# Kernel tuning notes

Measured on AMD Instinct MI355X. Metric: run time of the kernel, lower is better.

Reference implementation:

```python
import jax, jax.numpy as jnp
from jax import lax
import numpy as np

TWO_PI = 2.0 * np.pi

# ---- batched real-amplitude statevector simulator (RY/CNOT only -> real state) ----

def _init_state(batch, n):
    s = jnp.zeros((batch, 2 ** n), dtype=jnp.float32).at[:, 0].set(1.0)
    return s.reshape((batch,) + (2,) * n)

def _ry(state, wire, theta, n):
    # state: (B, 2,...,2); theta: scalar or (B,)
    ax = wire + 1
    h = theta * 0.5
    c = jnp.reshape(jnp.cos(h), (-1,) + (1,) * (n - 1))
    s = jnp.reshape(jnp.sin(h), (-1,) + (1,) * (n - 1))
    s0 = lax.index_in_dim(state, 0, ax, keepdims=False)
    s1 = lax.index_in_dim(state, 1, ax, keepdims=False)
    return jnp.stack([c * s0 - s * s1, s * s0 + c * s1], axis=ax)

def _cnot(state, ctrl, tgt):
    axc, axt = ctrl + 1, tgt + 1
    s0 = lax.index_in_dim(state, 0, axc, keepdims=True)
    s1 = lax.index_in_dim(state, 1, axc, keepdims=True)
    return jnp.concatenate([s0, jnp.flip(s1, axis=axt)], axis=axc)

def _expz(state, wire, n):
    sgn = jnp.reshape(jnp.array([1.0, -1.0], state.dtype),
                      (1,) * (wire + 1) + (2,) + (1,) * (n - wire - 1))
    return jnp.sum(state * state * sgn, axis=tuple(range(1, n + 1)))

# gate lists: ('ry', theta_index, wire) or ('cx', control, target)
EDGE_OPS = [('ry',0,0),('ry',1,1),('cx',0,1),('ry',2,2),('ry',3,3),('cx',3,2),
            ('ry',4,4),('ry',5,5),('cx',4,5),('ry',6,6),('ry',7,7),('cx',7,6),
            ('ry',8,1),('ry',9,2),('cx',1,2),('ry',10,5),('ry',11,6),('cx',6,5),
            ('ry',12,2),('ry',13,5),('cx',2,5),('ry',14,5)]

NODE_OPS = [('ry',0,0),('ry',1,1),('cx',0,1),('ry',2,2),('ry',3,3),('cx',3,2),
            ('ry',4,4),('ry',5,5),('cx',4,5),('ry',6,6),('ry',7,7),('cx',7,6),
            ('ry',8,8),('ry',9,9),('cx',8,9),('ry',10,10),('ry',11,11),('cx',11,10),
            ('ry',12,1),('ry',13,2),('cx',1,2),('ry',14,5),('ry',15,6),('cx',6,5),
            ('ry',16,9),('ry',17,10),('cx',10,9),('ry',18,2),('ry',19,5),('cx',2,5),
            ('ry',20,5),('ry',21,9),('cx',5,9),('ry',22,4)]

def _circuit(angles, theta, ops, n, meas_wire):
    st = _init_state(angles.shape[0], n)
    for i in range(n):  # input encoding RYs, per-sample angles
        st = _ry(st, i, angles[:, i], n)
    for op in ops:
        if op[0] == 'ry':
            st = _ry(st, op[2], theta[op[1]], n)
        else:
            st = _cnot(st, op[1], op[2])
    return _expz(st, meas_wire, n)

# ---- GNN pieces ----

def _edge_net(H, Ri, Ro, theta):
    bo = Ro.T @ H                      # [E,4]
    bi = Ri.T @ H                      # [E,4]
    B = jnp.concatenate([bo, bi], axis=1)  # [E,8]
    return (1.0 - _circuit(B, theta, EDGE_OPS, 8, 5)) * 0.5

def _node_net(H, e, Ri, Ro, theta):
    bo = Ro.T @ H                      # [E,4]
    bi = Ri.T @ H                      # [E,4]
    mi = (Ri * e[None, :]) @ bo        # [N,4]
    mo = (Ro * e[None, :]) @ bi        # [N,4]
    M = jnp.concatenate([mi, mo, H], axis=1)  # [N,12]
    return jnp.pi * (1.0 - _circuit(M, theta, NODE_OPS, 12, 9))

def _gnn(X, Ri, Ro, W_in, b_in, theta_edge, theta_node, n_iters=2):
    H = jnp.concatenate([jax.nn.sigmoid(X @ W_in + b_in) * TWO_PI, X], axis=1)  # [N,4]
    e = _edge_net(H, Ri, Ro, theta_edge)
    for _ in range(n_iters):
        h = _node_net(H, e, Ri, Ro, theta_node)   # [N]
        H = jnp.concatenate([h[:, None], X], axis=1)
        e = _edge_net(H, Ri, Ro, theta_edge)
    return e


def setup_inputs() -> dict:
    key = jax.random.key(0)
    ks = jax.random.split(key, 6)
    N, E = 2048, 4096
    X = jax.random.normal(ks[0], (N, 3), jnp.float32)
    recv = jax.random.randint(ks[1], (E,), 0, N)
    send = jax.random.randint(ks[2], (E,), 0, N)
    cols = jnp.arange(E)
    Ri = jnp.zeros((N, E), jnp.float32).at[recv, cols].set(1.0)
    Ro = jnp.zeros((N, E), jnp.float32).at[send, cols].set(1.0)
    W_in = jax.random.normal(ks[3], (3, 1), jnp.float32)
    b_in = jnp.zeros((1,), jnp.float32)
    theta_edge = jax.random.uniform(ks[4], (15,), jnp.float32, 0.0, TWO_PI)
    theta_node = jax.random.uniform(ks[5], (23,), jnp.float32, 0.0, TWO_PI)
    return {'X': X, 'Ri': Ri, 'Ro': Ro, 'W_in': W_in, 'b_in': b_in,
            'theta_edge': theta_edge, 'theta_node': theta_node}


def reference(X, Ri, Ro, W_in, b_in, theta_edge, theta_node):
    return _gnn(X, Ri, Ro, W_in, b_in, theta_edge, theta_node, n_iters=2)
```

## Files before the change

### kernel.cpp

```cpp
#include <hip/hip_runtime.h>
#include <math.h>

#define N_NODES 2048
#define N_EDGES 4096
#define PI_F 3.14159265358979323846f
#define TWO_PI_F 6.28318530717958647692f

__device__ __forceinline__ float agent_load(const float* p) {
    return __hip_atomic_load(p, __ATOMIC_RELAXED, __HIP_MEMORY_SCOPE_AGENT);
}
__device__ __forceinline__ void agent_store(float* p, float v) {
    __hip_atomic_store(p, v, __ATOMIC_RELAXED, __HIP_MEMORY_SCOPE_AGENT);
}
__device__ __forceinline__ void agent_store_i(int* p, int v) {
    __hip_atomic_store(p, v, __ATOMIC_RELAXED, __HIP_MEMORY_SCOPE_AGENT);
}
__device__ __forceinline__ void spin_ge(const int* p, int v) {
    while (__hip_atomic_load(p, __ATOMIC_RELAXED, __HIP_MEMORY_SCOPE_AGENT) < v)
        __builtin_amdgcn_s_sleep(2);
    asm volatile("" ::: "memory");
}


template<int M>
__device__ __forceinline__ void ry16(float* a, float c, float s) {
#pragma unroll
    for (int i = 0; i < 16; ++i)
        if (!(i & M)) {
            int j = i | M;
            float x0 = a[i], x1 = a[j];
            a[i] = c * x0 - s * x1;
            a[j] = s * x0 + c * x1;
        }
}
template<int MC, int MT>
__device__ __forceinline__ void cx16(float* a) {
#pragma unroll
    for (int i = 0; i < 16; ++i)
        if ((i & MC) && !(i & MT)) {
            int j = i | MT;
            float t = a[i]; a[i] = a[j]; a[j] = t;
        }
}

template<bool BTYPE>
__device__ __forceinline__ void sub16(const float* ic, const float* is,
                                      const float* thc, const float* ths,
                                      float& z, float& x) {
    float a[16];
    a[0] = ic[3]; a[1] = is[3];
#pragma unroll
    for (int i = 0; i < 2; ++i) { a[i | 2] = a[i] * is[2]; a[i] *= ic[2]; }
#pragma unroll
    for (int i = 0; i < 4; ++i) { a[i | 4] = a[i] * is[1]; a[i] *= ic[1]; }
#pragma unroll
    for (int i = 0; i < 8; ++i) { a[i | 8] = a[i] * is[0]; a[i] *= ic[0]; }
    ry16<8>(a, thc[0], ths[0]);
    ry16<4>(a, thc[1], ths[1]);
    cx16<8, 4>(a);
    ry16<2>(a, thc[2], ths[2]);
    ry16<1>(a, thc[3], ths[3]);
    cx16<1, 2>(a);
    ry16<4>(a, thc[4], ths[4]);
    ry16<2>(a, thc[5], ths[5]);
    if (BTYPE) { cx16<2, 4>(a); ry16<4>(a, thc[6], ths[6]); }
    else       { cx16<4, 2>(a); ry16<2>(a, thc[6], ths[6]); }
    const int m = BTYPE ? 4 : 2;
    z = 0.f; x = 0.f;
#pragma unroll
    for (int i = 0; i < 16; ++i) z += (i & m) ? -a[i] * a[i] : a[i] * a[i];
    if (BTYPE) {
#pragma unroll
        for (int i = 0; i < 16; ++i) if (!(i & 4)) x += a[i] * a[i | 4];
        x *= 2.f;
    }
}

__device__ __forceinline__ void edge_pub(
        float chh, float shh, const float* cxv, const float* sxv,
        const float* teC, const float* teS,
        float& zA, float& zB, float& xB) {
    float ic[4] = {chh, cxv[0], cxv[1], cxv[2]};
    float is[4] = {shh, sxv[0], sxv[1], sxv[2]};
    float dmy;
    {
        float thc[7] = {teC[0], teC[1], teC[2], teC[3], teC[8], teC[9], teC[12]};
        float ths[7] = {teS[0], teS[1], teS[2], teS[3], teS[8], teS[9], teS[12]};
        sub16<false>(ic, is, thc, ths, zA, dmy);
    }
    {
        float thc[7] = {teC[4], teC[5], teC[6], teC[7], teC[10], teC[11], teC[13]};
        float ths[7] = {teS[4], teS[5], teS[6], teS[7], teS[10], teS[11], teS[13]};
        sub16<true>(ic, is, thc, ths, zB, xB);
    }
}

__global__ __launch_bounds__(256) void k_setup(
        const float* __restrict__ X, const float* __restrict__ Ri,
        const float* __restrict__ Ro, const float* __restrict__ W,
        const float* __restrict__ b, const float* __restrict__ te,
        const float* __restrict__ tn,
        int* __restrict__ send, int* __restrict__ recv, float* __restrict__ H,
        float* __restrict__ pub, float* __restrict__ trig,
        int* __restrict__ deg) {
    int tid = blockIdx.x * blockDim.x + threadIdx.x;
    if (tid < N_NODES) {
        float x0 = X[tid*3+0], x1 = X[tid*3+1], x2 = X[tid*3+2];
        float z = x0*W[0] + x1*W[1] + x2*W[2] + b[0];
        float sg = 1.0f / (1.0f + __expf(-z));
        float h = sg * TWO_PI_F;
        ((float4*)H)[tid] = make_float4(h, x0, x1, x2);
        float chh, shh, cxv[3], sxv[3];
        __sincosf(0.5f*h,  &shh, &chh);
        __sincosf(0.5f*x0, &sxv[0], &cxv[0]);
        __sincosf(0.5f*x1, &sxv[1], &cxv[1]);
        __sincosf(0.5f*x2, &sxv[2], &cxv[2]);
        float teC[14], teS[14];
#pragma unroll
        for (int k = 0; k < 14; ++k) __sincosf(0.5f*te[k], &teS[k], &teC[k]);
        float zA, zB, xB;
        edge_pub(chh, shh, cxv, sxv, teC, teS, zA, zB, xB);
        pub[tid*4+0] = zA; pub[tid*4+1] = zB; pub[tid*4+2] = xB;
    }
    if (tid >= 4096 && tid < 4096 + 15) {
        int i = tid - 4096; float s, c;
        __sincosf(0.5f * te[i], &s, &c);
        trig[i] = c; trig[16 + i] = s;
    }
    if (tid >= 4224 && tid < 4224 + 23) {
        int i = tid - 4224; float s, c;
        __sincosf(0.5f * tn[i], &s, &c);
        trig[32 + i] = c; trig[56 + i] = s;
    }
    const float4 vi = ((const float4*)Ri)[tid];
    const float4 vo = ((const float4*)Ro)[tid];
    int base = tid * 4;
    int n = base >> 12;
    int e = base & (N_EDGES - 1);
    int cnt = 0;
    if (vi.x != 0.f) { recv[e+0] = n; ++cnt; }
    if (vi.y != 0.f) { recv[e+1] = n; ++cnt; }
    if (vi.z != 0.f) { recv[e+2] = n; ++cnt; }
    if (vi.w != 0.f) { recv[e+3] = n; ++cnt; }
    if (vo.x != 0.f) { send[e+0] = n; ++cnt; }
    if (vo.y != 0.f) { send[e+1] = n; ++cnt; }
    if (vo.z != 0.f) { send[e+2] = n; ++cnt; }
    if (vo.w != 0.f) { send[e+3] = n; ++cnt; }
    if (cnt) atomicAdd(&deg[n], cnt);
}

__device__ __forceinline__ void scatter8(float ev, const float4& Hs, const float4& Hr,
                                         int si, int ri,
                                         float* __restrict__ macc, int* __restrict__ arr) {
    atomicAdd(&macc[ri*8+0], ev*Hs.x); atomicAdd(&macc[ri*8+1], ev*Hs.y);
    atomicAdd(&macc[ri*8+2], ev*Hs.z); atomicAdd(&macc[ri*8+3], ev*Hs.w);
    atomicAdd(&macc[si*8+4], ev*Hr.x); atomicAdd(&macc[si*8+5], ev*Hr.y);
    atomicAdd(&macc[si*8+6], ev*Hr.z); atomicAdd(&macc[si*8+7], ev*Hr.w);
    asm volatile("s_waitcnt vmcnt(0)" ::: "memory");
    atomicAdd(&arr[ri], 1); atomicAdd(&arr[si], 1);
}

__global__ __launch_bounds__(64) void k_mega(
        float* __restrict__ H, float* __restrict__ pub,
        const int* __restrict__ send, const int* __restrict__ recv,
        const float* __restrict__ trig,
        float* __restrict__ maccA, float* __restrict__ maccB,
        int* __restrict__ arrA, int* __restrict__ arrB,
        int* __restrict__ epoch, const int* __restrict__ deg,
        float* __restrict__ out) {
    int lane = threadIdx.x;
    int blk  = blockIdx.x;

    if (blk < 64) {
        int e = blk * 64 + lane;
        int si = send[e], ri = recv[e];
        float4 Hs = ((const float4*)H)[si];
        float4 Hr = ((const float4*)H)[ri];
        float c14 = trig[14], s14 = trig[30];
        float C14 = c14*c14 - s14*s14;
        float S14 = 2.f*c14*s14;

        float zA = pub[si*4+0], zB = pub[ri*4+1], xB = pub[ri*4+2];
        float ev = 0.5f*(1.f - (C14*zA*zB - S14*xB));
        scatter8(ev, Hs, Hr, si, ri, maccA, arrA);

        spin_ge(epoch + si, 1); spin_ge(epoch + ri, 1);
        zA = agent_load(&pub[si*4+0]);
        zB = agent_load(&pub[ri*4+1]);
        xB = agent_load(&pub[ri*4+2]);
        Hs.x = agent_load(&H[si*4]);
        Hr.x = agent_load(&H[ri*4]);
        ev = 0.5f*(1.f - (C14*zA*zB - S14*xB));
        scatter8(ev, Hs, Hr, si, ri, maccB, arrB);

        spin_ge(epoch + si, 2); spin_ge(epoch + ri, 2);
        zA = agent_load(&pub[si*4+0]);
        zB = agent_load(&pub[ri*4+1]);
        xB = agent_load(&pub[ri*4+2]);
        out[e] = 0.5f*(1.f - (C14*zA*zB - S14*xB));
    } else {
        int n = (blk - 64) * 64 + lane;
        float4 Hn = ((const float4*)H)[n];
        float chh, shh, cxv[3], sxv[3];
        __sincosf(0.5f*Hn.x, &shh, &chh);
        __sincosf(0.5f*Hn.y, &sxv[0], &cxv[0]);
        __sincosf(0.5f*Hn.z, &sxv[1], &cxv[1]);
        __sincosf(0.5f*Hn.w, &sxv[2], &cxv[2]);
        int dg = deg[n];
        const float* teC = trig;      const float* teS = trig + 16;
        const float* tnC = trig + 32; const float* tnS = trig + 56;
        float C20 = tnC[20]*tnC[20] - tnS[20]*tnS[20];
        float S20 = 2.f*tnC[20]*tnS[20];

        for (int it = 0; it < 2; ++it) {
            const float* mc_ = it ? maccB : maccA;
            const int*   ar  = it ? arrB  : arrA;
            spin_ge(ar + n, dg);
            float M[8], mC[8], mS[8];
#pragma unroll
            for (int k = 0; k < 8; ++k) M[k] = agent_load(mc_ + n*8 + k);
#pragma unroll
            for (int k = 0; k < 8; ++k) __sincosf(0.5f*M[k], &mS[k], &mC[k]);
            float zA1, zA2, xA2, zB9, dmy;
            {
                float thc[7] = {tnC[0],tnC[1],tnC[2],tnC[3],tnC[12],tnC[13],tnC[18]};
                float ths[7] = {tnS[0],tnS[1],tnS[2],tnS[3],tnS[12],tnS[13],tnS[18]};
                sub16<false>(&mC[0], &mS[0], thc, ths, zA1, dmy);
            }
            {
                float thc[7] = {tnC[4],tnC[5],tnC[6],tnC[7],tnC[14],tnC[15],tnC[19]};
                float ths[7] = {tnS[4],tnS[5],tnS[6],tnS[7],tnS[14],tnS[15],tnS[19]};
                sub16<true>(&mC[4], &mS[4], thc, ths, zA2, xA2);
            }
            {
                float ic[4] = {chh, cxv[0], cxv[1], cxv[2]};
                float is[4] = {shh, sxv[0], sxv[1], sxv[2]};
                float thc[7] = {tnC[8],tnC[9],tnC[10],tnC[11],tnC[16],tnC[17],tnC[21]};
                float ths[7] = {tnS[8],tnS[9],tnS[10],tnS[11],tnS[16],tnS[17],tnS[21]};
                sub16<true>(ic, is, thc, ths, zB9, dmy);
            }
            float p9 = (C20*zA1*zA2 - S20*xA2) * zB9;
            float h = PI_F * (1.f - p9);
            __sincosf(0.5f*h, &shh, &chh);
            float zAe, zBe, xBe;
            edge_pub(chh, shh, cxv, sxv, teC, teS, zAe, zBe, xBe);
            agent_store(&pub[n*4+0], zAe);
            agent_store(&pub[n*4+1], zBe);
            agent_store(&pub[n*4+2], xBe);
            agent_store(&H[n*4], h);
            asm volatile("s_waitcnt vmcnt(0)" ::: "memory");
            agent_store_i(epoch + n, it + 1);
        }
    }
}

extern "C" void kernel_launch(void* const* d_in, const int* in_sizes, int n_in,
                              void* d_out, int out_size, void* d_ws, size_t ws_size,
                              hipStream_t stream) {
    const float* X  = (const float*)d_in[0];
    const float* Ri = (const float*)d_in[1];
    const float* Ro = (const float*)d_in[2];
    const float* W  = (const float*)d_in[3];
    const float* b  = (const float*)d_in[4];
    const float* te = (const float*)d_in[5];
    const float* tn = (const float*)d_in[6];
    float* out = (float*)d_out;

    int*   send  = (int*)d_ws;
    int*   recv  = send + N_EDGES;
    float* H     = (float*)(recv + N_EDGES);
    float* pub   = H + N_NODES * 4;
    float* trig  = pub + N_NODES * 4;
    float* maccA = trig + 128;
    float* maccB = maccA + N_NODES * 8;
    int*   arrA  = (int*)(maccB + N_NODES * 8);
    int*   arrB  = arrA + N_NODES;
    int*   epoch = arrB + N_NODES;
    int*   deg   = epoch + N_NODES;
    size_t zbytes = (size_t)(2 * N_NODES * 8 + 4 * N_NODES) * sizeof(float);

    hipMemsetAsync((void*)maccA, 0, zbytes, stream);
    int total4 = (N_NODES * N_EDGES) / 4;
    k_setup<<<total4 / 256, 256, 0, stream>>>(X, Ri, Ro, W, b, te, tn,
                                              send, recv, H, pub, trig, deg);
    k_mega<<<96, 64, 0, stream>>>(H, pub, send, recv, trig,
                                  maccA, maccB, arrA, arrB, epoch, deg, out);
}
```

Measured before the change: 123.5 us.

## Fuse setup scan and message-passing into one persistent dataflow kernel

Merges the adjacency-scan setup kernel and the persistent edge/node kernel into a single 256-block launch. Edge blocks spin on per-edge send/recv indices (stored as row+1) and per-node init flags, so message passing starts while the dense Ri/Ro scan is still running. Node blocks compute the initial features and trig values locally and wait on a global scan-done counter before reading degrees. This removes a kernel boundary and overlaps the bandwidth-bound scan with the start of the dependent work. In exchange the scan now runs from a fixed grid of persistent blocks with an unrolled strided loop, and correctness depends on all blocks being co-resident for the spin-waits.

```diff
diff --git a/kernel.cpp b/kernel.cpp
--- a/kernel.cpp
+++ b/kernel.cpp
@@ -6,7 +6,17 @@
 #define PI_F 3.14159265358979323846f
 #define TWO_PI_F 6.28318530717958647692f
 
+#define EDGE_BLKS 16
+#define NODE_BLKS 8
+#define TOTAL_BLKS 256
+#define SCAN_BLKS (TOTAL_BLKS - EDGE_BLKS)
+#define SCAN_STRIDE (SCAN_BLKS * 256)
+#define TOT4 (N_NODES * N_EDGES / 4)
+
 __device__ __forceinline__ float agent_load(const float* p) {
+    return __hip_atomic_load(p, __ATOMIC_RELAXED, __HIP_MEMORY_SCOPE_AGENT);
+}
+__device__ __forceinline__ int agent_load_i(const int* p) {
     return __hip_atomic_load(p, __ATOMIC_RELAXED, __HIP_MEMORY_SCOPE_AGENT);
 }
 __device__ __forceinline__ void agent_store(float* p, float v) {
@@ -19,6 +29,12 @@
     while (__hip_atomic_load(p, __ATOMIC_RELAXED, __HIP_MEMORY_SCOPE_AGENT) < v)
         __builtin_amdgcn_s_sleep(2);
     asm volatile("" ::: "memory");
+}
+__device__ __forceinline__ int spin_idx(const int* p) {
+    int v;
+    while ((v = agent_load_i(p)) == 0) __builtin_amdgcn_s_sleep(2);
+    asm volatile("" ::: "memory");
+    return v - 1;
 }
 
 
@@ -95,60 +111,6 @@
     }
 }
 
-__global__ __launch_bounds__(256) void k_setup(
-        const float* __restrict__ X, const float* __restrict__ Ri,
-        const float* __restrict__ Ro, const float* __restrict__ W,
-        const float* __restrict__ b, const float* __restrict__ te,
-        const float* __restrict__ tn,
-        int* __restrict__ send, int* __restrict__ recv, float* __restrict__ H,
-        float* __restrict__ pub, float* __restrict__ trig,
-        int* __restrict__ deg) {
-    int tid = blockIdx.x * blockDim.x + threadIdx.x;
-    if (tid < N_NODES) {
-        float x0 = X[tid*3+0], x1 = X[tid*3+1], x2 = X[tid*3+2];
-        float z = x0*W[0] + x1*W[1] + x2*W[2] + b[0];
-        float sg = 1.0f / (1.0f + __expf(-z));
-        float h = sg * TWO_PI_F;
-        ((float4*)H)[tid] = make_float4(h, x0, x1, x2);
-        float chh, shh, cxv[3], sxv[3];
-        __sincosf(0.5f*h,  &shh, &chh);
-        __sincosf(0.5f*x0, &sxv[0], &cxv[0]);
-        __sincosf(0.5f*x1, &sxv[1], &cxv[1]);
-        __sincosf(0.5f*x2, &sxv[2], &cxv[2]);
-        float teC[14], teS[14];
-#pragma unroll
-        for (int k = 0; k < 14; ++k) __sincosf(0.5f*te[k], &teS[k], &teC[k]);
-        float zA, zB, xB;
-        edge_pub(chh, shh, cxv, sxv, teC, teS, zA, zB, xB);
-        pub[tid*4+0] = zA; pub[tid*4+1] = zB; pub[tid*4+2] = xB;
-    }
-    if (tid >= 4096 && tid < 4096 + 15) {
-        int i = tid - 4096; float s, c;
-        __sincosf(0.5f * te[i], &s, &c);
-        trig[i] = c; trig[16 + i] = s;
-    }
-    if (tid >= 4224 && tid < 4224 + 23) {
-        int i = tid - 4224; float s, c;
-        __sincosf(0.5f * tn[i], &s, &c);
-        trig[32 + i] = c; trig[56 + i] = s;
-    }
-    const float4 vi = ((const float4*)Ri)[tid];
-    const float4 vo = ((const float4*)Ro)[tid];
-    int base = tid * 4;
-    int n = base >> 12;
-    int e = base & (N_EDGES - 1);
-    int cnt = 0;
-    if (vi.x != 0.f) { recv[e+0] = n; ++cnt; }
-    if (vi.y != 0.f) { recv[e+1] = n; ++cnt; }
-    if (vi.z != 0.f) { recv[e+2] = n; ++cnt; }
-    if (vi.w != 0.f) { recv[e+3] = n; ++cnt; }
-    if (vo.x != 0.f) { send[e+0] = n; ++cnt; }
-    if (vo.y != 0.f) { send[e+1] = n; ++cnt; }
-    if (vo.z != 0.f) { send[e+2] = n; ++cnt; }
-    if (vo.w != 0.f) { send[e+3] = n; ++cnt; }
-    if (cnt) atomicAdd(&deg[n], cnt);
-}
-
 __device__ __forceinline__ void scatter8(float ev, const float4& Hs, const float4& Hr,
                                          int si, int ri,
                                          float* __restrict__ macc, int* __restrict__ arr) {
@@ -160,27 +122,40 @@
     atomicAdd(&arr[ri], 1); atomicAdd(&arr[si], 1);
 }
 
-__global__ __launch_bounds__(64) void k_mega(
+__global__ __launch_bounds__(256, 1) void k_fused(
+        const float* __restrict__ X, const float* __restrict__ Ri,
+        const float* __restrict__ Ro, const float* __restrict__ W,
+        const float* __restrict__ b, const float* __restrict__ te,
+        const float* __restrict__ tn,
         float* __restrict__ H, float* __restrict__ pub,
-        const int* __restrict__ send, const int* __restrict__ recv,
-        const float* __restrict__ trig,
+        int* __restrict__ send, int* __restrict__ recv,
         float* __restrict__ maccA, float* __restrict__ maccB,
         int* __restrict__ arrA, int* __restrict__ arrB,
-        int* __restrict__ epoch, const int* __restrict__ deg,
+        int* __restrict__ epoch, int* __restrict__ inited,
+        int* __restrict__ deg, int* __restrict__ sdone,
         float* __restrict__ out) {
-    int lane = threadIdx.x;
-    int blk  = blockIdx.x;
-
-    if (blk < 64) {
-        int e = blk * 64 + lane;
-        int si = send[e], ri = recv[e];
-        float4 Hs = ((const float4*)H)[si];
-        float4 Hr = ((const float4*)H)[ri];
-        float c14 = trig[14], s14 = trig[30];
-        float C14 = c14*c14 - s14*s14;
-        float S14 = 2.f*c14*s14;
-
-        float zA = pub[si*4+0], zB = pub[ri*4+1], xB = pub[ri*4+2];
+    int blk = blockIdx.x, tid = threadIdx.x;
+
+    if (blk < EDGE_BLKS) {
+        int e = blk * 256 + tid;
+        float c14h, s14h;
+        __sincosf(0.5f * te[14], &s14h, &c14h);
+        float C14 = c14h*c14h - s14h*s14h;
+        float S14 = 2.f*c14h*s14h;
+
+        int si = spin_idx(send + e);
+        int ri = spin_idx(recv + e);
+        spin_ge(inited + si, 1);
+        spin_ge(inited + ri, 1);
+        float4 Hs, Hr;
+        Hs.x = agent_load(H+si*4+0); Hs.y = agent_load(H+si*4+1);
+        Hs.z = agent_load(H+si*4+2); Hs.w = agent_load(H+si*4+3);
+        Hr.x = agent_load(H+ri*4+0); Hr.y = agent_load(H+ri*4+1);
+        Hr.z = agent_load(H+ri*4+2); Hr.w = agent_load(H+ri*4+3);
+
+        float zA = agent_load(&pub[si*4+0]);
+        float zB = agent_load(&pub[ri*4+1]);
+        float xB = agent_load(&pub[ri*4+2]);
         float ev = 0.5f*(1.f - (C14*zA*zB - S14*xB));
         scatter8(ev, Hs, Hr, si, ri, maccA, arrA);
 
@@ -198,59 +173,119 @@
         zB = agent_load(&pub[ri*4+1]);
         xB = agent_load(&pub[ri*4+2]);
         out[e] = 0.5f*(1.f - (C14*zA*zB - S14*xB));
-    } else {
-        int n = (blk - 64) * 64 + lane;
-        float4 Hn = ((const float4*)H)[n];
-        float chh, shh, cxv[3], sxv[3];
-        __sincosf(0.5f*Hn.x, &shh, &chh);
-        __sincosf(0.5f*Hn.y, &sxv[0], &cxv[0]);
-        __sincosf(0.5f*Hn.z, &sxv[1], &cxv[1]);
-        __sincosf(0.5f*Hn.w, &sxv[2], &cxv[2]);
-        int dg = deg[n];
-        const float* teC = trig;      const float* teS = trig + 16;
-        const float* tnC = trig + 32; const float* tnS = trig + 56;
-        float C20 = tnC[20]*tnC[20] - tnS[20]*tnS[20];
-        float S20 = 2.f*tnC[20]*tnS[20];
-
-        for (int it = 0; it < 2; ++it) {
-            const float* mc_ = it ? maccB : maccA;
-            const int*   ar  = it ? arrB  : arrA;
-            spin_ge(ar + n, dg);
-            float M[8], mC[8], mS[8];
-#pragma unroll
-            for (int k = 0; k < 8; ++k) M[k] = agent_load(mc_ + n*8 + k);
-#pragma unroll
-            for (int k = 0; k < 8; ++k) __sincosf(0.5f*M[k], &mS[k], &mC[k]);
-            float zA1, zA2, xA2, zB9, dmy;
-            {
-                float thc[7] = {tnC[0],tnC[1],tnC[2],tnC[3],tnC[12],tnC[13],tnC[18]};
-                float ths[7] = {tnS[0],tnS[1],tnS[2],tnS[3],tnS[12],tnS[13],tnS[18]};
-                sub16<false>(&mC[0], &mS[0], thc, ths, zA1, dmy);
+        return;
+    }
+
+    bool is_node = (blk < EDGE_BLKS + NODE_BLKS);
+    int n = (blk - EDGE_BLKS) * 256 + tid;
+    float chh, shh, cxv[3], sxv[3];
+    float teC[14], teS[14], tnC[22], tnS[22];
+    if (is_node) {
+        float x0 = X[n*3+0], x1 = X[n*3+1], x2 = X[n*3+2];
+        float z = x0*W[0] + x1*W[1] + x2*W[2] + b[0];
+        float sg = 1.0f / (1.0f + __expf(-z));
+        float h = sg * TWO_PI_F;
+        __sincosf(0.5f*h,  &shh, &chh);
+        __sincosf(0.5f*x0, &sxv[0], &cxv[0]);
+        __sincosf(0.5f*x1, &sxv[1], &cxv[1]);
+        __sincosf(0.5f*x2, &sxv[2], &cxv[2]);
+#pragma unroll
+        for (int k = 0; k < 14; ++k) __sincosf(0.5f*te[k], &teS[k], &teC[k]);
+#pragma unroll
+        for (int k = 0; k < 22; ++k) __sincosf(0.5f*tn[k], &tnS[k], &tnC[k]);
+        float zA, zB, xB;
+        edge_pub(chh, shh, cxv, sxv, teC, teS, zA, zB, xB);
+        agent_store(&pub[n*4+0], zA);
+        agent_store(&pub[n*4+1], zB);
+        agent_store(&pub[n*4+2], xB);
+        agent_store(&H[n*4+0], h);
+        agent_store(&H[n*4+1], x0);
+        agent_store(&H[n*4+2], x2 == x2 ? x1 : x1);
+        agent_store(&H[n*4+3], x2);
+        asm volatile("s_waitcnt vmcnt(0)" ::: "memory");
+        agent_store_i(inited + n, 1);
+    }
+
+    {
+        int gid = (blk - EDGE_BLKS) * 256 + tid;
+        const float4* Ri4 = (const float4*)Ri;
+        const float4* Ro4 = (const float4*)Ro;
+        for (int t0 = gid; t0 < TOT4; t0 += 4 * SCAN_STRIDE) {
+            float4 vi[4], vo[4];
+#pragma unroll
+            for (int u = 0; u < 4; ++u) {
+                int t = t0 + u * SCAN_STRIDE;
+                if (t < TOT4) { vi[u] = Ri4[t]; vo[u] = Ro4[t]; }
             }
-            {
-                float thc[7] = {tnC[4],tnC[5],tnC[6],tnC[7],tnC[14],tnC[15],tnC[19]};
-                float ths[7] = {tnS[4],tnS[5],tnS[6],tnS[7],tnS[14],tnS[15],tnS[19]};
-                sub16<true>(&mC[4], &mS[4], thc, ths, zA2, xA2);
+#pragma unroll
+            for (int u = 0; u < 4; ++u) {
+                int t = t0 + u * SCAN_STRIDE;
+                if (t < TOT4) {
+                    int base = t * 4;
+                    int row = base >> 12;
+                    int e   = base & (N_EDGES - 1);
+                    int cnt = 0;
+                    if (vi[u].x != 0.f) { agent_store_i(recv+e+0, row+1); ++cnt; }
+                    if (vi[u].y != 0.f) { agent_store_i(recv+e+1, row+1); ++cnt; }
+                    if (vi[u].z != 0.f) { agent_store_i(recv+e+2, row+1); ++cnt; }
+                    if (vi[u].w != 0.f) { agent_store_i(recv+e+3, row+1); ++cnt; }
+                    if (vo[u].x != 0.f) { agent_store_i(send+e+0, row+1); ++cnt; }
+                    if (vo[u].y != 0.f) { agent_store_i(send+e+1, row+1); ++cnt; }
+                    if (vo[u].z != 0.f) { agent_store_i(send+e+2, row+1); ++cnt; }
+                    if (vo[u].w != 0.f) { agent_store_i(send+e+3, row+1); ++cnt; }
+                    if (cnt) atomicAdd(&deg[row], cnt);
+                }
             }
-            {
-                float ic[4] = {chh, cxv[0], cxv[1], cxv[2]};
-                float is[4] = {shh, sxv[0], sxv[1], sxv[2]};
-                float thc[7] = {tnC[8],tnC[9],tnC[10],tnC[11],tnC[16],tnC[17],tnC[21]};
-                float ths[7] = {tnS[8],tnS[9],tnS[10],tnS[11],tnS[16],tnS[17],tnS[21]};
-                sub16<true>(ic, is, thc, ths, zB9, dmy);
-            }
-            float p9 = (C20*zA1*zA2 - S20*xA2) * zB9;
-            float h = PI_F * (1.f - p9);
-            __sincosf(0.5f*h, &shh, &chh);
-            float zAe, zBe, xBe;
-            edge_pub(chh, shh, cxv, sxv, teC, teS, zAe, zBe, xBe);
-            agent_store(&pub[n*4+0], zAe);
-            agent_store(&pub[n*4+1], zBe);
-            agent_store(&pub[n*4+2], xBe);
-            agent_store(&H[n*4], h);
-            asm volatile("s_waitcnt vmcnt(0)" ::: "memory");
-            agent_store_i(epoch + n, it + 1);
-        }
+        }
+        asm volatile("s_waitcnt vmcnt(0)" ::: "memory");
+        __syncthreads();
+        if (tid == 0) atomicAdd(sdone, 1);
+    }
+    if (!is_node) return;
+
+    spin_ge(sdone, SCAN_BLKS);
+    int dg = agent_load_i(deg + n);
+    float C20 = tnC[20]*tnC[20] - tnS[20]*tnS[20];
+    float S20 = 2.f*tnC[20]*tnS[20];
+
+    for (int it = 0; it < 2; ++it) {
+        const float* mc_ = it ? maccB : maccA;
+        const int*   ar  = it ? arrB  : arrA;
+        spin_ge(ar + n, dg);
+        float M[8], mC[8], mS[8];
+#pragma unroll
+        for (int k = 0; k < 8; ++k) M[k] = agent_load(mc_ + n*8 + k);
+#pragma unroll
+        for (int k = 0; k < 8; ++k) __sincosf(0.5f*M[k], &mS[k], &mC[k]);
+        float zA1, zA2, xA2, zB9, dmy;
+        {
+            float thc[7] = {tnC[0],tnC[1],tnC[2],tnC[3],tnC[12],tnC[13],tnC[18]};
+            float ths[7] = {tnS[0],tnS[1],tnS[2],tnS[3],tnS[12],tnS[13],tnS[18]};
+            sub16<false>(&mC[0], &mS[0], thc, ths, zA1, dmy);
+        }
+        {
+            float thc[7] = {tnC[4],tnC[5],tnC[6],tnC[7],tnC[14],tnC[15],tnC[19]};
+            float ths[7] = {tnS[4],tnS[5],tnS[6],tnS[7],tnS[14],tnS[15],tnS[19]};
+            sub16<true>(&mC[4], &mS[4], thc, ths, zA2, xA2);
+        }
+        {
+            float ic[4] = {chh, cxv[0], cxv[1], cxv[2]};
+            float is[4] = {shh, sxv[0], sxv[1], sxv[2]};
+            float thc[7] = {tnC[8],tnC[9],tnC[10],tnC[11],tnC[16],tnC[17],tnC[21]};
+            float ths[7] = {tnS[8],tnS[9],tnS[10],tnS[11],tnS[16],tnS[17],tnS[21]};
+            sub16<true>(ic, is, thc, ths, zB9, dmy);
+        }
+        float p9 = (C20*zA1*zA2 - S20*xA2) * zB9;
+        float h = PI_F * (1.f - p9);
+        __sincosf(0.5f*h, &shh, &chh);
+        float zAe, zBe, xBe;
+        edge_pub(chh, shh, cxv, sxv, teC, teS, zAe, zBe, xBe);
+        agent_store(&pub[n*4+0], zAe);
+        agent_store(&pub[n*4+1], zBe);
+        agent_store(&pub[n*4+2], xBe);
+        agent_store(&H[n*4], h);
+        asm volatile("s_waitcnt vmcnt(0)" ::: "memory");
+        agent_store_i(epoch + n, it + 1);
     }
 }
 
@@ -266,23 +301,23 @@
     const float* tn = (const float*)d_in[6];
     float* out = (float*)d_out;
 
-    int*   send  = (int*)d_ws;
+    float* H     = (float*)d_ws;
+    float* pub   = H + N_NODES * 4;
+    int*   send  = (int*)(pub + N_NODES * 4);
     int*   recv  = send + N_EDGES;
-    float* H     = (float*)(recv + N_EDGES);
-    float* pub   = H + N_NODES * 4;
-    float* trig  = pub + N_NODES * 4;
-    float* maccA = trig + 128;
+    float* maccA = (float*)(recv + N_EDGES);
     float* maccB = maccA + N_NODES * 8;
     int*   arrA  = (int*)(maccB + N_NODES * 8);
     int*   arrB  = arrA + N_NODES;
     int*   epoch = arrB + N_NODES;
-    int*   deg   = epoch + N_NODES;
-    size_t zbytes = (size_t)(2 * N_NODES * 8 + 4 * N_NODES) * sizeof(float);
-
-    hipMemsetAsync((void*)maccA, 0, zbytes, stream);
-    int total4 = (N_NODES * N_EDGES) / 4;
-    k_setup<<<total4 / 256, 256, 0, stream>>>(X, Ri, Ro, W, b, te, tn,
-                                              send, recv, H, pub, trig, deg);
-    k_mega<<<96, 64, 0, stream>>>(H, pub, send, recv, trig,
-                                  maccA, maccB, arrA, arrB, epoch, deg, out);
-}
+    int*   inited= epoch + N_NODES;
+    int*   deg   = inited + N_NODES;
+    int*   sdone = deg + N_NODES;
+    size_t zbytes = (size_t)(2*N_EDGES + 4*N_NODES*8 + 5*N_NODES + 16) * 4;
+
+    hipMemsetAsync((void*)send, 0, zbytes, stream);
+    k_fused<<<TOTAL_BLKS, 256, 0, stream>>>(X, Ri, Ro, W, b, te, tn,
+                                            H, pub, send, recv,
+                                            maccA, maccB, arrA, arrB,
+                                            epoch, inited, deg, sdone, out);
+}
```

Measured after the change: 137.3 us. 11.2% more time.

## Compute final node update redundantly in edge threads to drop a sync stage

Applied to the files above, without the earlier changes.

Edge threads now wait directly on the second-iteration message accumulators of their sender and receiver nodes. Each edge thread recomputes the final node update and edge-publish circuits for both endpoints itself, instead of waiting for node blocks to publish epoch 2. Node blocks run only the first iteration, and the input-dependent node subcircuit is hoisted ahead of the first spin-wait. This removes one cross-block handoff from the critical path. In exchange each edge thread does two full node circuit evaluations, duplicating work across edges that share a node.

```diff
diff --git a/kernel.cpp b/kernel.cpp
--- a/kernel.cpp
+++ b/kernel.cpp
@@ -7,6 +7,9 @@
 #define TWO_PI_F 6.28318530717958647692f
 
 __device__ __forceinline__ float agent_load(const float* p) {
+    return __hip_atomic_load(p, __ATOMIC_RELAXED, __HIP_MEMORY_SCOPE_AGENT);
+}
+__device__ __forceinline__ int agent_load_i(const int* p) {
     return __hip_atomic_load(p, __ATOMIC_RELAXED, __HIP_MEMORY_SCOPE_AGENT);
 }
 __device__ __forceinline__ void agent_store(float* p, float v) {
@@ -76,23 +79,65 @@
     }
 }
 
+__device__ __forceinline__ float pubA(float chh, float shh,
+                                      const float* cxv, const float* sxv,
+                                      const float* teC, const float* teS) {
+    float ic[4] = {chh, cxv[0], cxv[1], cxv[2]};
+    float is[4] = {shh, sxv[0], sxv[1], sxv[2]};
+    float thc[7] = {teC[0], teC[1], teC[2], teC[3], teC[8], teC[9], teC[12]};
+    float ths[7] = {teS[0], teS[1], teS[2], teS[3], teS[8], teS[9], teS[12]};
+    float z, x;
+    sub16<false>(ic, is, thc, ths, z, x);
+    return z;
+}
+__device__ __forceinline__ void pubB(float chh, float shh,
+                                     const float* cxv, const float* sxv,
+                                     const float* teC, const float* teS,
+                                     float& z, float& x) {
+    float ic[4] = {chh, cxv[0], cxv[1], cxv[2]};
+    float is[4] = {shh, sxv[0], sxv[1], sxv[2]};
+    float thc[7] = {teC[4], teC[5], teC[6], teC[7], teC[10], teC[11], teC[13]};
+    float ths[7] = {teS[4], teS[5], teS[6], teS[7], teS[10], teS[11], teS[13]};
+    sub16<true>(ic, is, thc, ths, z, x);
+}
 __device__ __forceinline__ void edge_pub(
         float chh, float shh, const float* cxv, const float* sxv,
         const float* teC, const float* teS,
         float& zA, float& zB, float& xB) {
-    float ic[4] = {chh, cxv[0], cxv[1], cxv[2]};
-    float is[4] = {shh, sxv[0], sxv[1], sxv[2]};
-    float dmy;
+    zA = pubA(chh, shh, cxv, sxv, teC, teS);
+    pubB(chh, shh, cxv, sxv, teC, teS, zB, xB);
+}
+
+__device__ __forceinline__ float node_update(
+        const float* M, float& chh, float& shh,
+        const float* cxv, const float* sxv,
+        const float* tnC, const float* tnS, float C20, float S20) {
+    float zB9, dmy;
     {
-        float thc[7] = {teC[0], teC[1], teC[2], teC[3], teC[8], teC[9], teC[12]};
-        float ths[7] = {teS[0], teS[1], teS[2], teS[3], teS[8], teS[9], teS[12]};
-        sub16<false>(ic, is, thc, ths, zA, dmy);
-    }
+        float ic[4] = {chh, cxv[0], cxv[1], cxv[2]};
+        float is[4] = {shh, sxv[0], sxv[1], sxv[2]};
+        float thc[7] = {tnC[8],tnC[9],tnC[10],tnC[11],tnC[16],tnC[17],tnC[21]};
+        float ths[7] = {tnS[8],tnS[9],tnS[10],tnS[11],tnS[16],tnS[17],tnS[21]};
+        sub16<true>(ic, is, thc, ths, zB9, dmy);
+    }
+    float mC[8], mS[8];
+#pragma unroll
+    for (int k = 0; k < 8; ++k) __sincosf(0.5f * M[k], &mS[k], &mC[k]);
+    float zA1, zA2, xA2;
     {
-        float thc[7] = {teC[4], teC[5], teC[6], teC[7], teC[10], teC[11], teC[13]};
-        float ths[7] = {teS[4], teS[5], teS[6], teS[7], teS[10], teS[11], teS[13]};
-        sub16<true>(ic, is, thc, ths, zB, xB);
-    }
+        float thc[7] = {tnC[0],tnC[1],tnC[2],tnC[3],tnC[12],tnC[13],tnC[18]};
+        float ths[7] = {tnS[0],tnS[1],tnS[2],tnS[3],tnS[12],tnS[13],tnS[18]};
+        sub16<false>(&mC[0], &mS[0], thc, ths, zA1, dmy);
+    }
+    {
+        float thc[7] = {tnC[4],tnC[5],tnC[6],tnC[7],tnC[14],tnC[15],tnC[19]};
+        float ths[7] = {tnS[4],tnS[5],tnS[6],tnS[7],tnS[14],tnS[15],tnS[19]};
+        sub16<true>(&mC[4], &mS[4], thc, ths, zA2, xA2);
+    }
+    float p9 = (C20*zA1*zA2 - S20*xA2) * zB9;
+    float h = PI_F * (1.f - p9);
+    __sincosf(0.5f*h, &shh, &chh);
+    return h;
 }
 
 __global__ __launch_bounds__(256) void k_setup(
@@ -170,15 +215,27 @@
         float* __restrict__ out) {
     int lane = threadIdx.x;
     int blk  = blockIdx.x;
+    const float* teC = trig;      const float* teS = trig + 16;
+    const float* tnC = trig + 32; const float* tnS = trig + 56;
 
     if (blk < 64) {
         int e = blk * 64 + lane;
         int si = send[e], ri = recv[e];
+        int dgs = deg[si], dgr = deg[ri];
         float4 Hs = ((const float4*)H)[si];
         float4 Hr = ((const float4*)H)[ri];
         float c14 = trig[14], s14 = trig[30];
         float C14 = c14*c14 - s14*s14;
         float S14 = 2.f*c14*s14;
+        float C20 = tnC[20]*tnC[20] - tnS[20]*tnS[20];
+        float S20 = 2.f*tnC[20]*tnS[20];
+        float cxs[3], sxs[3], cxr[3], sxr[3];
+        __sincosf(0.5f*Hs.y, &sxs[0], &cxs[0]);
+        __sincosf(0.5f*Hs.z, &sxs[1], &cxs[1]);
+        __sincosf(0.5f*Hs.w, &sxs[2], &cxs[2]);
+        __sincosf(0.5f*Hr.y, &sxr[0], &cxr[0]);
+        __sincosf(0.5f*Hr.z, &sxr[1], &cxr[1]);
+        __sincosf(0.5f*Hr.w, &sxr[2], &cxr[2]);
 
         float zA = pub[si*4+0], zB = pub[ri*4+1], xB = pub[ri*4+2];
         float ev = 0.5f*(1.f - (C14*zA*zB - S14*xB));
@@ -188,15 +245,28 @@
         zA = agent_load(&pub[si*4+0]);
         zB = agent_load(&pub[ri*4+1]);
         xB = agent_load(&pub[ri*4+2]);
-        Hs.x = agent_load(&H[si*4]);
-        Hr.x = agent_load(&H[ri*4]);
+        float h1s = agent_load(&H[si*4]);
+        float h1r = agent_load(&H[ri*4]);
+        Hs.x = h1s; Hr.x = h1r;
         ev = 0.5f*(1.f - (C14*zA*zB - S14*xB));
         scatter8(ev, Hs, Hr, si, ri, maccB, arrB);
 
-        spin_ge(epoch + si, 2); spin_ge(epoch + ri, 2);
-        zA = agent_load(&pub[si*4+0]);
-        zB = agent_load(&pub[ri*4+1]);
-        xB = agent_load(&pub[ri*4+2]);
+        float ch1s, sh1s, ch1r, sh1r;
+        __sincosf(0.5f*h1s, &sh1s, &ch1s);
+        __sincosf(0.5f*h1r, &sh1r, &ch1r);
+
+        while (agent_load_i(arrB + si) < dgs || agent_load_i(arrB + ri) < dgr)
+            __builtin_amdgcn_s_sleep(1);
+        asm volatile("" ::: "memory");
+        float Ms[8], Mr[8];
+#pragma unroll
+        for (int k = 0; k < 8; ++k) Ms[k] = agent_load(maccB + si*8 + k);
+#pragma unroll
+        for (int k = 0; k < 8; ++k) Mr[k] = agent_load(maccB + ri*8 + k);
+        node_update(Ms, ch1s, sh1s, cxs, sxs, tnC, tnS, C20, S20);
+        node_update(Mr, ch1r, sh1r, cxr, sxr, tnC, tnS, C20, S20);
+        zA = pubA(ch1s, sh1s, cxs, sxs, teC, teS);
+        pubB(ch1r, sh1r, cxr, sxr, teC, teS, zB, xB);
         out[e] = 0.5f*(1.f - (C14*zA*zB - S14*xB));
     } else {
         int n = (blk - 64) * 64 + lane;
@@ -207,50 +277,45 @@
         __sincosf(0.5f*Hn.z, &sxv[1], &cxv[1]);
         __sincosf(0.5f*Hn.w, &sxv[2], &cxv[2]);
         int dg = deg[n];
-        const float* teC = trig;      const float* teS = trig + 16;
-        const float* tnC = trig + 32; const float* tnS = trig + 56;
         float C20 = tnC[20]*tnC[20] - tnS[20]*tnS[20];
         float S20 = 2.f*tnC[20]*tnS[20];
 
-        for (int it = 0; it < 2; ++it) {
-            const float* mc_ = it ? maccB : maccA;
-            const int*   ar  = it ? arrB  : arrA;
-            spin_ge(ar + n, dg);
-            float M[8], mC[8], mS[8];
-#pragma unroll
-            for (int k = 0; k < 8; ++k) M[k] = agent_load(mc_ + n*8 + k);
-#pragma unroll
-            for (int k = 0; k < 8; ++k) __sincosf(0.5f*M[k], &mS[k], &mC[k]);
-            float zA1, zA2, xA2, zB9, dmy;
-            {
-                float thc[7] = {tnC[0],tnC[1],tnC[2],tnC[3],tnC[12],tnC[13],tnC[18]};
-                float ths[7] = {tnS[0],tnS[1],tnS[2],tnS[3],tnS[12],tnS[13],tnS[18]};
-                sub16<false>(&mC[0], &mS[0], thc, ths, zA1, dmy);
-            }
-            {
-                float thc[7] = {tnC[4],tnC[5],tnC[6],tnC[7],tnC[14],tnC[15],tnC[19]};
-                float ths[7] = {tnS[4],tnS[5],tnS[6],tnS[7],tnS[14],tnS[15],tnS[19]};
-                sub16<true>(&mC[4], &mS[4], thc, ths, zA2, xA2);
-            }
-            {
-                float ic[4] = {chh, cxv[0], cxv[1], cxv[2]};
-                float is[4] = {shh, sxv[0], sxv[1], sxv[2]};
-                float thc[7] = {tnC[8],tnC[9],tnC[10],tnC[11],tnC[16],tnC[17],tnC[21]};
-                float ths[7] = {tnS[8],tnS[9],tnS[10],tnS[11],tnS[16],tnS[17],tnS[21]};
-                sub16<true>(ic, is, thc, ths, zB9, dmy);
-            }
-            float p9 = (C20*zA1*zA2 - S20*xA2) * zB9;
-            float h = PI_F * (1.f - p9);
-            __sincosf(0.5f*h, &shh, &chh);
-            float zAe, zBe, xBe;
-            edge_pub(chh, shh, cxv, sxv, teC, teS, zAe, zBe, xBe);
-            agent_store(&pub[n*4+0], zAe);
-            agent_store(&pub[n*4+1], zBe);
-            agent_store(&pub[n*4+2], xBe);
-            agent_store(&H[n*4], h);
-            asm volatile("s_waitcnt vmcnt(0)" ::: "memory");
-            agent_store_i(epoch + n, it + 1);
-        }
+        float zB9, dmy;
+        {
+            float ic[4] = {chh, cxv[0], cxv[1], cxv[2]};
+            float is[4] = {shh, sxv[0], sxv[1], sxv[2]};
+            float thc[7] = {tnC[8],tnC[9],tnC[10],tnC[11],tnC[16],tnC[17],tnC[21]};
+            float ths[7] = {tnS[8],tnS[9],tnS[10],tnS[11],tnS[16],tnS[17],tnS[21]};
+            sub16<true>(ic, is, thc, ths, zB9, dmy);
+        }
+        spin_ge(arrA + n, dg);
+        float M[8], mC[8], mS[8];
+#pragma unroll
+        for (int k = 0; k < 8; ++k) M[k] = agent_load(maccA + n*8 + k);
+#pragma unroll
+        for (int k = 0; k < 8; ++k) __sincosf(0.5f*M[k], &mS[k], &mC[k]);
+        float zA1, zA2, xA2;
+        {
+            float thc[7] = {tnC[0],tnC[1],tnC[2],tnC[3],tnC[12],tnC[13],tnC[18]};
+            float ths[7] = {tnS[0],tnS[1],tnS[2],tnS[3],tnS[12],tnS[13],tnS[18]};
+            sub16<false>(&mC[0], &mS[0], thc, ths, zA1, dmy);
+        }
+        {
+            float thc[7] = {tnC[4],tnC[5],tnC[6],tnC[7],tnC[14],tnC[15],tnC[19]};
+            float ths[7] = {tnS[4],tnS[5],tnS[6],tnS[7],tnS[14],tnS[15],tnS[19]};
+            sub16<true>(&mC[4], &mS[4], thc, ths, zA2, xA2);
+        }
+        float p9 = (C20*zA1*zA2 - S20*xA2) * zB9;
+        float h = PI_F * (1.f - p9);
+        __sincosf(0.5f*h, &shh, &chh);
+        float zAe, zBe, xBe;
+        edge_pub(chh, shh, cxv, sxv, teC, teS, zAe, zBe, xBe);
+        agent_store(&pub[n*4+0], zAe);
+        agent_store(&pub[n*4+1], zBe);
+        agent_store(&pub[n*4+2], xBe);
+        agent_store(&H[n*4], h);
+        asm volatile("s_waitcnt vmcnt(0)" ::: "memory");
+        agent_store_i(epoch + n, 1);
     }
 }
 
```

Result: slower. 126.8 us (+2.7%).
